# Kernel optimization log

Hardware: AMD Instinct MI355X
Metric: run time of the kernel (lower is better)

## Reference

```python
import jax, jax.numpy as jnp
import numpy as np

B, S, D = 4, 4096, 1024
H = 8                    # num_heads
DK = D // H              # head_k_dim = 128
DV = D // H              # head_v_dim = 128
KLEPE = 5                # lepe kernel size
ROPE_BASE = 10000.0


def rotate_half(x):
    x1, x2 = jnp.split(x, 2, axis=-1)
    return jnp.concatenate([-x2, x1], axis=-1)


def rope_sin_cos(seq_len, dim):
    inv_freq = 1.0 / (ROPE_BASE ** (jnp.arange(0, dim, 2, dtype=jnp.float32) / dim))
    freqs = jnp.arange(seq_len, dtype=jnp.float32)[:, None] * inv_freq[None, :]
    emb = jnp.concatenate([freqs, freqs], axis=-1)  # [S, dim]
    return jnp.sin(emb), jnp.cos(emb)


def mala_attn(q, k, v):
    """Magnitude-aware linear attention with inline RoPE.

    Attention weights A_ij = (scale*q_i.k_j + 1) / (scale*q_i.(sum_j k_j) + S):
    rows sum to 1 but, unlike plain linear attention, the sharpness of the
    distribution still depends on ||q_i|| (magnitude rectification). Computed
    in O(S*d^2) linear form without materializing the SxS matrix.
    q, k: [B,S,H,DK]; v: [B,S,H,DV].
    """
    sin, cos = rope_sin_cos(q.shape[1], q.shape[-1])
    sin, cos = sin[None, :, None, :], cos[None, :, None, :]
    q = q * cos + rotate_half(q) * sin
    k = k * cos + rotate_half(k) * sin
    scale = q.shape[-1] ** -0.5
    seq_len = q.shape[1]
    kv = jnp.einsum('bshd,bshe->bhde', k, v)      # [B,H,DK,DV]
    ksum = k.sum(axis=1)                          # [B,H,DK]
    vsum = v.sum(axis=1)                          # [B,H,DV]
    num = jnp.einsum('bshd,bhde->bshe', q, kv) * scale + vsum[:, None, :, :]
    den = jnp.einsum('bshd,bhd->bsh', q, ksum) * scale + seq_len
    return num / den[..., None]


def lepe_conv(v, w, b):
    # depthwise Conv1d over the sequence axis; channel id = h*DV + d
    Bb, Ss = v.shape[0], v.shape[1]
    x = v.transpose(0, 2, 3, 1).reshape(Bb, H * DV, Ss)   # [B, C, S]
    y = jax.lax.conv_general_dilated(
        x, w, window_strides=(1,), padding=[(KLEPE // 2, KLEPE // 2)],
        dimension_numbers=('NCH', 'OIH', 'NCH'), feature_group_count=H * DV)
    y = y + b[None, :, None]
    return y.reshape(Bb, H, DV, Ss).transpose(0, 3, 1, 2)  # [B,S,H,DV]


def setup_inputs() -> dict:
    key = jax.random.key(0)
    ks = jax.random.split(key, 8)
    w = 0.02
    return {
        'hidden_states': jax.random.normal(ks[0], (B, S, D), dtype=jnp.float32),
        'Wq': jax.random.normal(ks[1], (D, D), dtype=jnp.float32) * w,
        'Wk': jax.random.normal(ks[2], (D, D), dtype=jnp.float32) * w,
        'Wv': jax.random.normal(ks[3], (D, D), dtype=jnp.float32) * w,
        'Wg': jax.random.normal(ks[4], (D, D), dtype=jnp.float32) * w,
        'Wo': jax.random.normal(ks[5], (D, D), dtype=jnp.float32) * w,
        'lepe_w': jax.random.normal(ks[6], (D, 1, KLEPE), dtype=jnp.float32) * 0.1,
        'lepe_b': jnp.zeros((D,), dtype=jnp.float32),
    }


def reference(hidden_states, Wq, Wk, Wv, Wg, Wo, lepe_w, lepe_b):
    Bb, Ss, _ = hidden_states.shape
    q = (hidden_states @ Wq.T).reshape(Bb, Ss, H, DK)
    k = (hidden_states @ Wk.T).reshape(Bb, Ss, H, DK)
    v = (hidden_states @ Wv.T).reshape(Bb, Ss, H, DV)
    o_gate = hidden_states @ Wg.T                          # [B,S,D]
    o = mala_attn(q, k, v) + lepe_conv(v, lepe_w, lepe_b)  # [B,S,H,DV]
    o = o.reshape(Bb, Ss, H * DV) * o_gate
    return o @ Wo.T
```

## Files before the change

kernel.cpp:

```cpp
#include <hip/hip_runtime.h>
#include <math.h>
#include <stdint.h>


typedef __bf16 bf16;
typedef __bf16 bf16x2 __attribute__((ext_vector_type(2)));
typedef __bf16 bf16x4 __attribute__((ext_vector_type(4)));
typedef __bf16 bf16x8 __attribute__((ext_vector_type(8)));
typedef float f32x4 __attribute__((ext_vector_type(4)));

static constexpr float kScale = 0.08838834764831845f;

__device__ __forceinline__ void async_copy16(const void* g, void* l) {
  __builtin_amdgcn_global_load_lds(
      (const __attribute__((address_space(1))) void*)(uintptr_t)g,
      (__attribute__((address_space(3))) void*)(uintptr_t)l, 16, 0, 0);
}

__global__ __launch_bounds__(512, 1) void gemm_qkvg(
    const bf16* __restrict__ A, const bf16* __restrict__ Bw,
    bf16* __restrict__ C, const float2* __restrict__ tab)
{
  __shared__ __align__(16) char smem[131072];

  const int t = threadIdx.x;
  const int bid = blockIdx.x;
  const int n = bid >> 3;
  const int bx = (bid & 7) * 8 + (n & 7);
  const int by = n >> 3;
  const long m0 = (long)bx * 256;
  const long n0 = (long)by * 256;

  const int d0 = t * 16;
  const int dd = d0 ^ (((d0 >> 7) & 7) << 4);
  const int rT = dd >> 7;
  const int cT = (dd & 127) >> 1;
  const bf16* aSt = A  + (m0 + rT) * 1024 + cT;
  const bf16* bSt = Bw + (n0 + rT) * 1024 + cT;
  char* ldsDst = smem + d0;

  const int lane = t & 63, wid = t >> 6;
  const int wm = wid >> 2, wn = wid & 3;
  const int fm = lane & 15, fq = lane >> 4;
  const int xsw = (fm & 7) << 4;
  const int o0 = (fq * 16) ^ xsw;
  const int o1 = o0 ^ 64;
  const char* ldsA0 = smem + wm * 16384 + fm * 128 + o0;
  const char* ldsA1 = smem + wm * 16384 + fm * 128 + o1;
  const char* ldsB0 = smem + 32768 + (wn >> 1) * 16384 +
                      ((wn & 1) * 64 + fm) * 128 + o0;
  const char* ldsB1 = ldsB0 + (o1 - o0);

  f32x4 acc[8][4] = {};
  bf16x8 a4[4][2], b4[4][2];

#define STAGE_A(kt, h) do {                                                  \
    const bf16* s_ = aSt + (long)(h) * 131072 + (kt) * 64;                   \
    char* d_ = ldsDst + ((kt) & 1) * 65536 + (h) * 16384;                    \
    async_copy16(s_, d_);                                                    \
    async_copy16(s_ + 65536, d_ + 8192);                                     \
  } while (0)
#define STAGE_B(kt, h) do {                                                  \
    const bf16* s_ = bSt + (long)(h) * 131072 + (kt) * 64;                   \
    char* d_ = ldsDst + ((kt) & 1) * 65536 + 32768 + (h) * 16384;            \
    async_copy16(s_, d_);                                                    \
    async_copy16(s_ + 65536, d_ + 8192);                                     \
  } while (0)
#define LOAD_A(buf, qi) do {                                                 \
    const char* p0_ = ldsA0 + (buf) * 65536 + (qi) * 8192;                   \
    const char* p1_ = ldsA1 + (buf) * 65536 + (qi) * 8192;                   \
    a4[0][0] = *(const bf16x8*)(p0_);                                        \
    a4[0][1] = *(const bf16x8*)(p1_);                                        \
    a4[1][0] = *(const bf16x8*)(p0_ + 2048);                                 \
    a4[1][1] = *(const bf16x8*)(p1_ + 2048);                                 \
    a4[2][0] = *(const bf16x8*)(p0_ + 4096);                                 \
    a4[2][1] = *(const bf16x8*)(p1_ + 4096);                                 \
    a4[3][0] = *(const bf16x8*)(p0_ + 6144);                                 \
    a4[3][1] = *(const bf16x8*)(p1_ + 6144);                                 \
  } while (0)
#define LOAD_B(buf, qj) do {                                                 \
    const char* p0_ = ldsB0 + (buf) * 65536 + (qj) * 4096;                   \
    const char* p1_ = ldsB1 + (buf) * 65536 + (qj) * 4096;                   \
    b4[2*(qj)+0][0] = *(const bf16x8*)(p0_);                                 \
    b4[2*(qj)+0][1] = *(const bf16x8*)(p1_);                                 \
    b4[2*(qj)+1][0] = *(const bf16x8*)(p0_ + 2048);                          \
    b4[2*(qj)+1][1] = *(const bf16x8*)(p1_ + 2048);                          \
  } while (0)
#define MM1(i, j, ks)                                                        \
    acc[i][j] = __builtin_amdgcn_mfma_f32_16x16x32_bf16(                     \
        a4[(i) & 3][ks], b4[j][ks], acc[i][j], 0, 0, 0)
#define MFMA_Q(qi, qj) do {                                                  \
    MM1(4*(qi)+0, 2*(qj)+0, 0); MM1(4*(qi)+1, 2*(qj)+0, 0);                  \
    MM1(4*(qi)+2, 2*(qj)+0, 0); MM1(4*(qi)+3, 2*(qj)+0, 0);                  \
    MM1(4*(qi)+0, 2*(qj)+1, 0); MM1(4*(qi)+1, 2*(qj)+1, 0);                  \
    MM1(4*(qi)+2, 2*(qj)+1, 0); MM1(4*(qi)+3, 2*(qj)+1, 0);                  \
    MM1(4*(qi)+0, 2*(qj)+0, 1); MM1(4*(qi)+1, 2*(qj)+0, 1);                  \
    MM1(4*(qi)+2, 2*(qj)+0, 1); MM1(4*(qi)+3, 2*(qj)+0, 1);                  \
    MM1(4*(qi)+0, 2*(qj)+1, 1); MM1(4*(qi)+1, 2*(qj)+1, 1);                  \
    MM1(4*(qi)+2, 2*(qj)+1, 1); MM1(4*(qi)+3, 2*(qj)+1, 1);                  \
  } while (0)
#define BAR()    __builtin_amdgcn_s_barrier()
#define SCHEDB() __builtin_amdgcn_sched_barrier(0)
#define PRIO(p)  __builtin_amdgcn_s_setprio(p)

  STAGE_A(0, 0); STAGE_A(0, 1); STAGE_B(0, 0); STAGE_B(0, 1);
  STAGE_B(1, 0); STAGE_B(1, 1); STAGE_A(1, 0); STAGE_A(1, 1);
  asm volatile("s_waitcnt vmcnt(8)" ::: "memory");
  BAR(); SCHEDB();

#pragma unroll 1
  for (int it = 0; it < 7; ++it) {
    const int k2 = 2 * it + 2;
    const int k3 = 2 * it + 3;
    LOAD_A(0, 0); LOAD_B(0, 0);
    BAR(); SCHEDB(); PRIO(1); MFMA_Q(0, 0); PRIO(0); BAR(); SCHEDB();
    LOAD_B(0, 1);
    BAR(); SCHEDB(); PRIO(1); MFMA_Q(0, 1); PRIO(0); BAR(); SCHEDB();
    LOAD_A(0, 1);
    STAGE_B(k2, 0);
    BAR(); SCHEDB(); PRIO(1); MFMA_Q(1, 1); PRIO(0); BAR(); SCHEDB();
    STAGE_B(k2, 1); STAGE_A(k2, 0); STAGE_A(k2, 1);
    BAR(); SCHEDB(); PRIO(1); MFMA_Q(1, 0); PRIO(0);
    asm volatile("s_waitcnt vmcnt(8)" ::: "memory");
    BAR(); SCHEDB();
    LOAD_A(1, 0); LOAD_B(1, 0);
    BAR(); SCHEDB(); PRIO(1); MFMA_Q(0, 0); PRIO(0); BAR(); SCHEDB();
    LOAD_B(1, 1);
    BAR(); SCHEDB(); PRIO(1); MFMA_Q(0, 1); PRIO(0); BAR(); SCHEDB();
    LOAD_A(1, 1);
    STAGE_B(k3, 0);
    BAR(); SCHEDB(); PRIO(1); MFMA_Q(1, 1); PRIO(0); BAR(); SCHEDB();
    STAGE_B(k3, 1); STAGE_A(k3, 0); STAGE_A(k3, 1);
    BAR(); SCHEDB(); PRIO(1); MFMA_Q(1, 0); PRIO(0);
    asm volatile("s_waitcnt vmcnt(8)" ::: "memory");
    BAR(); SCHEDB();
  }

  {
    LOAD_A(0, 0); LOAD_B(0, 0);
    BAR(); SCHEDB(); PRIO(1); MFMA_Q(0, 0); PRIO(0); BAR(); SCHEDB();
    LOAD_B(0, 1);
    BAR(); SCHEDB(); PRIO(1); MFMA_Q(0, 1); PRIO(0); BAR(); SCHEDB();
    LOAD_A(0, 1);
    BAR(); SCHEDB(); PRIO(1); MFMA_Q(1, 1); PRIO(0); BAR(); SCHEDB();
    BAR(); SCHEDB(); PRIO(1); MFMA_Q(1, 0); PRIO(0);
    asm volatile("s_waitcnt vmcnt(0)" ::: "memory");
    BAR(); SCHEDB();
    LOAD_A(1, 0); LOAD_B(1, 0);
    BAR(); SCHEDB(); PRIO(1); MFMA_Q(0, 0); PRIO(0); BAR(); SCHEDB();
    LOAD_B(1, 1);
    BAR(); SCHEDB(); PRIO(1); MFMA_Q(0, 1); PRIO(0); BAR(); SCHEDB();
    LOAD_A(1, 1);
    BAR(); SCHEDB(); PRIO(1); MFMA_Q(1, 1); PRIO(0); BAR(); SCHEDB();
    BAR(); SCHEDB(); PRIO(1); MFMA_Q(1, 0); PRIO(0); BAR(); SCHEDB();
  }

#undef STAGE_A
#undef STAGE_B
#undef LOAD_A
#undef LOAD_B
#undef MM1
#undef MFMA_Q
#undef BAR
#undef SCHEDB
#undef PRIO

  bf16* T = (bf16*)smem;
  __syncthreads();
#pragma unroll 1
  for (int hw = 0; hw < 2; ++hw) {
    if (wm == hw) {
#pragma unroll
      for (int rf = 0; rf < 8; ++rf)
#pragma unroll
        for (int cf = 0; cf < 4; ++cf)
#pragma unroll
          for (int r = 0; r < 4; ++r)
            T[(rf * 16 + fq * 4 + r) * 264 + wn * 64 + cf * 16 + fm] =
                (bf16)acc[rf][cf][r];
    }
    __syncthreads();
    if (by < 8) {
#pragma unroll
      for (int ii = 0; ii < 32; ++ii) {
        const int pi = t + ii * 512;
        const int row = pi >> 7, pr = pi & 127;
        const int hd = pr >> 6, i = pr & 63;
        const int c0 = hd * 128 + i;
        const int s = (int)((m0 + hw * 128 + row) & 4095);
        const float2 sc = tab[s * 64 + i];
        float x1 = (float)T[row * 264 + c0];
        float x2 = (float)T[row * 264 + c0 + 64];
        T[row * 264 + c0]      = (bf16)(x1 * sc.y - x2 * sc.x);
        T[row * 264 + c0 + 64] = (bf16)(x2 * sc.y + x1 * sc.x);
      }
      __syncthreads();
    }
#pragma unroll
    for (int ii = 0; ii < 8; ++ii) {
      const int cid = t + ii * 512;
      const int row = cid >> 5, ch = cid & 31;
      *(bf16x8*)(C + (m0 + hw * 128 + row) * 4096 + n0 + ch * 8) =
          *(const bf16x8*)(T + row * 264 + ch * 8);
    }
    __syncthreads();
  }
}

__global__ __launch_bounds__(256, 2) void gemm_final(
    const bf16* __restrict__ A, const bf16* __restrict__ Bw,
    float* __restrict__ C)
{
  __shared__ __align__(16) bf16 As[128 * 32];
  __shared__ __align__(16) bf16 Bs[128 * 32];
  const int t = threadIdx.x;
  const int bid = blockIdx.x;
  const int xcd = bid & 7, n = bid >> 3;
  const int bx = xcd * 16 + (n & 15);
  const int by = n >> 4;
  const long m0 = (long)bx * 128;
  A  += m0 * 1024;
  Bw += (long)by * 131072;
  C  += m0 * 1024 + (long)by * 128;

  const int i0 = t, i1 = t + 256;
  const bf16* gA0 = A  + (long)(i0 >> 2) * 1024 + (i0 & 3) * 8;
  const bf16* gA1 = A  + (long)(i1 >> 2) * 1024 + (i1 & 3) * 8;
  const bf16* gB0 = Bw + (long)(i0 >> 2) * 1024 + (i0 & 3) * 8;
  const bf16* gB1 = Bw + (long)(i1 >> 2) * 1024 + (i1 & 3) * 8;
  bf16* lA0 = As + i0 * 8; bf16* lA1 = As + i1 * 8;
  bf16* lB0 = Bs + i0 * 8; bf16* lB1 = Bs + i1 * 8;

  const int lane = t & 63, wv = t >> 6;
  const int moff = (wv & 1) * 64, noff = (wv >> 1) * 64;
  const int fm = lane & 15, fq = lane >> 4;

  f32x4 acc[4][4] = {};

  for (int k0 = 0; k0 < 1024; k0 += 32) {
    async_copy16(gA0, lA0); async_copy16(gA1, lA1);
    async_copy16(gB0, lB0); async_copy16(gB1, lB1);
    gA0 += 32; gA1 += 32; gB0 += 32; gB1 += 32;
    __syncthreads();
    bf16x8 af[4], bfv[4];
#pragma unroll
    for (int i = 0; i < 4; ++i) {
      af[i]  = *(const bf16x8*)(As + (moff + i * 16 + fm) * 32 + fq * 8);
      bfv[i] = *(const bf16x8*)(Bs + (noff + i * 16 + fm) * 32 + fq * 8);
    }
#pragma unroll
    for (int i = 0; i < 4; ++i)
#pragma unroll
      for (int j = 0; j < 4; ++j)
        acc[i][j] = __builtin_amdgcn_mfma_f32_16x16x32_bf16(af[i], bfv[j], acc[i][j], 0, 0, 0);
    __syncthreads();
  }

#pragma unroll
  for (int i = 0; i < 4; ++i)
#pragma unroll
    for (int j = 0; j < 4; ++j)
#pragma unroll
      for (int r = 0; r < 4; ++r)
        C[(long)(moff + i * 16 + fq * 4 + r) * 1024 + noff + j * 16 + fm] = acc[i][j][r];
}

__global__ __launch_bounds__(256, 2) void gemm_num(
    const bf16* __restrict__ QKVG, const bf16* __restrict__ kvTall,
    const float* __restrict__ ksum, const float* __restrict__ vsum,
    const float* __restrict__ lepe_w, const float* __restrict__ lepe_b,
    bf16* __restrict__ obuf)
{
  __shared__ __align__(16) char smem[17408];
  bf16* As = (bf16*)smem;
  bf16* Bs = (bf16*)(smem + 8192);
  bf16* T  = (bf16*)smem;
  __shared__ float sden[128], svsum[128], slb[128], sksum[128];
  __shared__ float slw[5][128];

  const int t = threadIdx.x;
  const int h = blockIdx.y, b = blockIdx.z;
  const int bh = b * 8 + h;
  const long m0 = (long)blockIdx.x * 128;
  const bf16* A  = QKVG + (long)b * 16777216 + m0 * 4096 + h * 128;
  const bf16* Bw = kvTall + (long)bh * 16384;

  if (t < 128) {
    sksum[t] = ksum[bh * 128 + t];
    svsum[t] = vsum[bh * 128 + t];
    slb[t]   = lepe_b[h * 128 + t];
#pragma unroll
    for (int j = 0; j < 5; ++j) slw[j][t] = lepe_w[(h * 128 + t) * 5 + j];
  }

  const int i0 = t, i1 = t + 256;
  const bf16* gA0 = A + (long)(i0 >> 2) * 4096 + (i0 & 3) * 8;
  const bf16* gA1 = A + (long)(i1 >> 2) * 4096 + (i1 & 3) * 8;
  const bf16* gB0 = Bw + (long)(i0 >> 2) * 128 + (i0 & 3) * 8;
  const bf16* gB1 = Bw + (long)(i1 >> 2) * 128 + (i1 & 3) * 8;
  bf16* lA0 = As + i0 * 8; bf16* lA1 = As + i1 * 8;
  bf16* lB0 = Bs + i0 * 8; bf16* lB1 = Bs + i1 * 8;

  const int lane = t & 63, wv = t >> 6;
  const int moff = (wv & 1) * 64, noff = (wv >> 1) * 64;
  const int fm = lane & 15, fq = lane >> 4;

  f32x4 acc[4][4] = {};
  float dacc = 0.f;

  for (int k0 = 0; k0 < 128; k0 += 32) {
    async_copy16(gA0, lA0); async_copy16(gA1, lA1);
    async_copy16(gB0, lB0); async_copy16(gB1, lB1);
    gA0 += 32; gA1 += 32; gB0 += 32; gB1 += 32;
    __syncthreads();
    bf16x8 af[4], bfv[4];
#pragma unroll
    for (int i = 0; i < 4; ++i) {
      af[i]  = *(const bf16x8*)(As + (moff + i * 16 + fm) * 32 + fq * 8);
      bfv[i] = *(const bf16x8*)(Bs + (noff + i * 16 + fm) * 32 + fq * 8);
    }
#pragma unroll
    for (int i = 0; i < 4; ++i)
#pragma unroll
      for (int j = 0; j < 4; ++j)
        acc[i][j] = __builtin_amdgcn_mfma_f32_16x16x32_bf16(af[i], bfv[j], acc[i][j], 0, 0, 0);
    if (t < 128) {
#pragma unroll
      for (int c8 = 0; c8 < 4; ++c8) {
        bf16x8 q8 = *(const bf16x8*)(As + t * 32 + c8 * 8);
#pragma unroll
        for (int e = 0; e < 8; ++e) dacc += (float)q8[e] * sksum[k0 + c8 * 8 + e];
      }
    }
    __syncthreads();
  }
  if (t < 128) sden[t] = dacc * kScale + 4096.0f;

  const int c2 = lane * 2;
  const float w0[5] = {slw[0][c2], slw[1][c2], slw[2][c2], slw[3][c2], slw[4][c2]};
  const float w1[5] = {slw[0][c2+1], slw[1][c2+1], slw[2][c2+1], slw[3][c2+1], slw[4][c2+1]};
  const float lb0 = slb[c2], lb1 = slb[c2 + 1];

#pragma unroll
  for (int half = 0; half < 2; ++half) {
    if ((wv & 1) == half) {
#pragma unroll
      for (int i = 0; i < 4; ++i)
#pragma unroll
        for (int j = 0; j < 4; ++j)
#pragma unroll
          for (int r = 0; r < 4; ++r) {
            const int col = noff + j * 16 + fm;
            T[(i * 16 + fq * 4 + r) * 136 + col] = (bf16)(acc[i][j][r] * kScale + svsum[col]);
          }
    }
    __syncthreads();
    for (int rr = 0; rr < 16; ++rr) {
      const int lrow = wv * 16 + rr;
      const int row = half * 64 + lrow;
      const int s = (int)(m0 + row);
      const long grow = (long)b * 4096 + s;
      const float rden = 1.0f / sden[row];
      const bf16* vrow = QKVG + grow * 4096 + 2048 + h * 128 + c2;
      bf16x2 a2 = *(const bf16x2*)(T + lrow * 136 + c2);
      float lep0 = lb0, lep1 = lb1;
#pragma unroll
      for (int jt = 0; jt < 5; ++jt) {
        const int srow = s + jt - 2;
        if (srow >= 0 && srow < 4096) {
          bf16x2 v2 = *(const bf16x2*)(vrow + (long)(jt - 2) * 4096);
          lep0 += (float)v2[0] * w0[jt];
          lep1 += (float)v2[1] * w1[jt];
        }
      }
      bf16x2 g2 = *(const bf16x2*)(QKVG + grow * 4096 + 3072 + h * 128 + c2);
      bf16x2 o2;
      o2[0] = (bf16)(((float)a2[0] * rden + lep0) * (float)g2[0]);
      o2[1] = (bf16)(((float)a2[1] * rden + lep1) * (float)g2[1]);
      *(bf16x2*)(obuf + grow * 1024 + h * 128 + c2) = o2;
    }
    __syncthreads();
  }
}

__global__ void prep_kernel(const float* __restrict__ X, const float* __restrict__ Wq,
                            const float* __restrict__ Wk, const float* __restrict__ Wv,
                            const float* __restrict__ Wg, const float* __restrict__ Wo,
                            bf16* __restrict__ Xb, bf16* __restrict__ Wcat,
                            bf16* __restrict__ Wob, float2* __restrict__ tab)
{
  const int blk = blockIdx.x;
  if (blk < 16384) {
    long g = ((long)blk * 256 + threadIdx.x) * 4;
    float4 v = *(const float4*)(X + g);
    bf16x4 o = {(bf16)v.x, (bf16)v.y, (bf16)v.z, (bf16)v.w};
    *(bf16x4*)(Xb + g) = o;
  } else if (blk < 21504) {
    long g = ((long)(blk - 16384) * 256 + threadIdx.x) * 4;
    if (g < 4194304) {
      long idx = g & 1048575;
      int sel = (int)(g >> 20);
      const float* s = sel == 0 ? Wq : sel == 1 ? Wk : sel == 2 ? Wv : Wg;
      float4 v = *(const float4*)(s + idx);
      bf16x4 o = {(bf16)v.x, (bf16)v.y, (bf16)v.z, (bf16)v.w};
      *(bf16x4*)(Wcat + g) = o;
    } else {
      long idx = g - 4194304;
      float4 v = *(const float4*)(Wo + idx);
      bf16x4 o = {(bf16)v.x, (bf16)v.y, (bf16)v.z, (bf16)v.w};
      *(bf16x4*)(Wob + idx) = o;
    }
  } else {
    int idx = (blk - 21504) * 256 + threadIdx.x;
    int s = idx >> 6, i = idx & 63;
    float inv = powf(10000.0f, -((float)(2 * i)) / 128.0f);
    float ang = (float)s * inv;
    float sn, cs;
    sincosf(ang, &sn, &cs);
    tab[idx] = make_float2(sn, cs);
  }
}

__global__ __launch_bounds__(256, 2) void kv_mfma(
    const bf16* __restrict__ QKVG, float* __restrict__ kvp,
    float* __restrict__ ksump, float* __restrict__ vsump)
{
  __shared__ __align__(16) bf16 VT[128 * 40];
  __shared__ __align__(16) bf16 KT[128 * 40];
  const int t = threadIdx.x;
  const int chunk = blockIdx.x, bh = blockIdx.y;
  const int b = bh >> 3, h = bh & 7;
  const long rowbase = ((long)b * 4096 + chunk * 256) * 4096 + h * 128;
  const bf16* Kg = QKVG + rowbase + 1024;
  const bf16* Vg = QKVG + rowbase + 2048;

  const int sp = t >> 4, fc = t & 15;
  const int lane = t & 63, wv = t >> 6;
  const int eoff = (wv & 1) * 64, doff = (wv >> 1) * 64;
  const int fm = lane & 15, fq = lane >> 4;
  const int srow = t & 127;
  const bool sumK = t >= 128;

  f32x4 acc[4][4] = {};
  float rsum = 0.f;

  for (int sb = 0; sb < 256; sb += 32) {
    const long go = (long)(sb + 2 * sp) * 4096 + fc * 8;
    bf16x8 v0 = *(const bf16x8*)(Vg + go);
    bf16x8 v1 = *(const bf16x8*)(Vg + go + 4096);
    bf16x8 k0 = *(const bf16x8*)(Kg + go);
    bf16x8 k1 = *(const bf16x8*)(Kg + go + 4096);
#pragma unroll
    for (int j = 0; j < 8; ++j) {
      const int f = fc * 8 + j;
      bf16x2 vp2 = {v0[j], v1[j]};
      bf16x2 kp2 = {k0[j], k1[j]};
      *(bf16x2*)(VT + f * 40 + 2 * sp) = vp2;
      *(bf16x2*)(KT + f * 40 + 2 * sp) = kp2;
    }
    __syncthreads();
    bf16x8 af[4], bfv[4];
#pragma unroll
    for (int i = 0; i < 4; ++i) {
      af[i]  = *(const bf16x8*)(VT + (eoff + i * 16 + fm) * 40 + fq * 8);
      bfv[i] = *(const bf16x8*)(KT + (doff + i * 16 + fm) * 40 + fq * 8);
    }
#pragma unroll
    for (int i = 0; i < 4; ++i)
#pragma unroll
      for (int j = 0; j < 4; ++j)
        acc[i][j] = __builtin_amdgcn_mfma_f32_16x16x32_bf16(af[i], bfv[j], acc[i][j], 0, 0, 0);
    const bf16* rp = (sumK ? KT : VT) + srow * 40;
#pragma unroll
    for (int i = 0; i < 4; ++i) {
      bf16x8 r8 = *(const bf16x8*)(rp + i * 8);
#pragma unroll
      for (int j = 0; j < 8; ++j) rsum += (float)r8[j];
    }
    __syncthreads();
  }

  float* plane = kvp + ((long)chunk * 32 + bh) * 16384;
#pragma unroll
  for (int i = 0; i < 4; ++i)
#pragma unroll
    for (int j = 0; j < 4; ++j)
#pragma unroll
      for (int r = 0; r < 4; ++r)
        plane[(long)(eoff + i * 16 + fq * 4 + r) * 128 + (doff + j * 16 + fm)] = acc[i][j][r];
  float* sdst = (sumK ? ksump : vsump) + ((long)chunk * 32 + bh) * 128 + srow;
  *sdst = rsum;
}

__global__ void kv_reduce(const float* __restrict__ kvp, const float* __restrict__ ksump,
                          const float* __restrict__ vsump, bf16* __restrict__ kvT,
                          float* __restrict__ ksum, float* __restrict__ vsum)
{
  long g = (long)blockIdx.x * 256 + threadIdx.x;
  long bh = g >> 14, idx = g & 16383;
  float s = 0.f;
#pragma unroll
  for (int c = 0; c < 16; ++c) s += kvp[((long)c * 32 + bh) * 16384 + idx];
  kvT[g] = (bf16)s;
  if (g < 8192) {
    int bh2 = (int)(g >> 8), rem = (int)(g & 255), f = rem & 127;
    const float* src = (rem >> 7) ? ksump : vsump;
    float* dst = (rem >> 7) ? ksum : vsum;
    float s2 = 0.f;
#pragma unroll
    for (int c = 0; c < 16; ++c) s2 += src[((long)c * 32 + bh2) * 128 + f];
    dst[bh2 * 128 + f] = s2;
  }
}

extern "C" void kernel_launch(void* const* d_in, const int* in_sizes, int n_in,
                              void* d_out, int out_size, void* d_ws, size_t ws_size,
                              hipStream_t stream)
{
  const float* X      = (const float*)d_in[0];
  const float* Wq     = (const float*)d_in[1];
  const float* Wk     = (const float*)d_in[2];
  const float* Wv     = (const float*)d_in[3];
  const float* Wg     = (const float*)d_in[4];
  const float* Wo     = (const float*)d_in[5];
  const float* lepe_w = (const float*)d_in[6];
  const float* lepe_b = (const float*)d_in[7];
  float* out = (float*)d_out;

  char* ws = (char*)d_ws;
  bf16*   Xb    = (bf16*)(ws);
  float*  kvp   = (float*)(ws);
  bf16*   Wcat  = (bf16*)(ws + 33554432);
  bf16*   Wob   = (bf16*)(ws + 41943040);
  float2* tab   = (float2*)(ws + 44040192);
  float*  ksump = (float*)(ws + 44040192);
  float*  vsump = (float*)(ws + 44302336);
  bf16*   QKVG  = (bf16*)(ws + 46137344);
  float*  ksum  = (float*)(ws + 180355072);
  float*  vsum  = (float*)(ws + 180371456);
  bf16*   kvT   = (bf16*)(ws + 180387840);
  bf16*   obuf  = (bf16*)(ws + 181960704);

  prep_kernel<<<22528, 256, 0, stream>>>(X, Wq, Wk, Wv, Wg, Wo, Xb, Wcat, Wob, tab);

  gemm_qkvg<<<1024, 512, 0, stream>>>(Xb, Wcat, QKVG, tab);

  kv_mfma<<<dim3(16, 32), 256, 0, stream>>>(QKVG, kvp, ksump, vsump);
  kv_reduce<<<2048, 256, 0, stream>>>(kvp, ksump, vsump, kvT, ksum, vsum);

  gemm_num<<<dim3(32, 8, 4), 256, 0, stream>>>(QKVG, kvT, ksum, vsum, lepe_w, lepe_b, obuf);

  gemm_final<<<1024, 256, 0, stream>>>(obuf, Wob, out);
}
```

Measured before the change: 432.1 us.

## Restructure QKVG GEMM main loop with separate A-fragment registers and fewer barriers

```diff
diff --git a/kernel.cpp b/kernel.cpp
--- a/kernel.cpp
+++ b/kernel.cpp
@@ -52,7 +52,7 @@
   const char* ldsB1 = ldsB0 + (o1 - o0);
 
   f32x4 acc[8][4] = {};
-  bf16x8 a4[4][2], b4[4][2];
+  bf16x8 aLo[4][2], aHi[4][2], b4[4][2];
 
 #define STAGE_A(kt, h) do {                                                  \
     const bf16* s_ = aSt + (long)(h) * 131072 + (kt) * 64;                   \
@@ -66,17 +66,17 @@
     async_copy16(s_, d_);                                                    \
     async_copy16(s_ + 65536, d_ + 8192);                                     \
   } while (0)
-#define LOAD_A(buf, qi) do {                                                 \
+#define LOAD_A(dst, buf, qi) do {                                            \
     const char* p0_ = ldsA0 + (buf) * 65536 + (qi) * 8192;                   \
     const char* p1_ = ldsA1 + (buf) * 65536 + (qi) * 8192;                   \
-    a4[0][0] = *(const bf16x8*)(p0_);                                        \
-    a4[0][1] = *(const bf16x8*)(p1_);                                        \
-    a4[1][0] = *(const bf16x8*)(p0_ + 2048);                                 \
-    a4[1][1] = *(const bf16x8*)(p1_ + 2048);                                 \
-    a4[2][0] = *(const bf16x8*)(p0_ + 4096);                                 \
-    a4[2][1] = *(const bf16x8*)(p1_ + 4096);                                 \
-    a4[3][0] = *(const bf16x8*)(p0_ + 6144);                                 \
-    a4[3][1] = *(const bf16x8*)(p1_ + 6144);                                 \
+    dst[0][0] = *(const bf16x8*)(p0_);                                       \
+    dst[0][1] = *(const bf16x8*)(p1_);                                       \
+    dst[1][0] = *(const bf16x8*)(p0_ + 2048);                                \
+    dst[1][1] = *(const bf16x8*)(p1_ + 2048);                                \
+    dst[2][0] = *(const bf16x8*)(p0_ + 4096);                                \
+    dst[2][1] = *(const bf16x8*)(p1_ + 4096);                                \
+    dst[3][0] = *(const bf16x8*)(p0_ + 6144);                                \
+    dst[3][1] = *(const bf16x8*)(p1_ + 6144);                                \
   } while (0)
 #define LOAD_B(buf, qj) do {                                                 \
     const char* p0_ = ldsB0 + (buf) * 65536 + (qj) * 4096;                   \
@@ -86,22 +86,32 @@
     b4[2*(qj)+1][0] = *(const bf16x8*)(p0_ + 2048);                          \
     b4[2*(qj)+1][1] = *(const bf16x8*)(p1_ + 2048);                          \
   } while (0)
-#define MM1(i, j, ks)                                                        \
+#define MM1(arr, i, j, ks)                                                   \
     acc[i][j] = __builtin_amdgcn_mfma_f32_16x16x32_bf16(                     \
-        a4[(i) & 3][ks], b4[j][ks], acc[i][j], 0, 0, 0)
-#define MFMA_Q(qi, qj) do {                                                  \
-    MM1(4*(qi)+0, 2*(qj)+0, 0); MM1(4*(qi)+1, 2*(qj)+0, 0);                  \
-    MM1(4*(qi)+2, 2*(qj)+0, 0); MM1(4*(qi)+3, 2*(qj)+0, 0);                  \
-    MM1(4*(qi)+0, 2*(qj)+1, 0); MM1(4*(qi)+1, 2*(qj)+1, 0);                  \
-    MM1(4*(qi)+2, 2*(qj)+1, 0); MM1(4*(qi)+3, 2*(qj)+1, 0);                  \
-    MM1(4*(qi)+0, 2*(qj)+0, 1); MM1(4*(qi)+1, 2*(qj)+0, 1);                  \
-    MM1(4*(qi)+2, 2*(qj)+0, 1); MM1(4*(qi)+3, 2*(qj)+0, 1);                  \
-    MM1(4*(qi)+0, 2*(qj)+1, 1); MM1(4*(qi)+1, 2*(qj)+1, 1);                  \
-    MM1(4*(qi)+2, 2*(qj)+1, 1); MM1(4*(qi)+3, 2*(qj)+1, 1);                  \
+        arr[(i) & 3][ks], b4[j][ks], acc[i][j], 0, 0, 0)
+#define MFMA_Q(arr, qi, qj) do {                                             \
+    MM1(arr, 4*(qi)+0, 2*(qj)+0, 0); MM1(arr, 4*(qi)+1, 2*(qj)+0, 0);        \
+    MM1(arr, 4*(qi)+2, 2*(qj)+0, 0); MM1(arr, 4*(qi)+3, 2*(qj)+0, 0);        \
+    MM1(arr, 4*(qi)+0, 2*(qj)+1, 0); MM1(arr, 4*(qi)+1, 2*(qj)+1, 0);        \
+    MM1(arr, 4*(qi)+2, 2*(qj)+1, 0); MM1(arr, 4*(qi)+3, 2*(qj)+1, 0);        \
+    MM1(arr, 4*(qi)+0, 2*(qj)+0, 1); MM1(arr, 4*(qi)+1, 2*(qj)+0, 1);        \
+    MM1(arr, 4*(qi)+2, 2*(qj)+0, 1); MM1(arr, 4*(qi)+3, 2*(qj)+0, 1);        \
+    MM1(arr, 4*(qi)+0, 2*(qj)+1, 1); MM1(arr, 4*(qi)+1, 2*(qj)+1, 1);        \
+    MM1(arr, 4*(qi)+2, 2*(qj)+1, 1); MM1(arr, 4*(qi)+3, 2*(qj)+1, 1);        \
   } while (0)
 #define BAR()    __builtin_amdgcn_s_barrier()
 #define SCHEDB() __builtin_amdgcn_sched_barrier(0)
 #define PRIO(p)  __builtin_amdgcn_s_setprio(p)
+#define TILE_HEAD(buf) do {                                                  \
+    LOAD_A(aLo, buf, 0);                                                     \
+    LOAD_B(buf, 0); LOAD_B(buf, 1);                                          \
+    LOAD_A(aHi, buf, 1);                                                     \
+    PRIO(1);                                                                 \
+    MFMA_Q(aLo, 0, 0); MFMA_Q(aLo, 0, 1); MFMA_Q(aHi, 1, 1);                 \
+    PRIO(0);                                                                 \
+    asm volatile("s_waitcnt lgkmcnt(0)" ::: "memory");                       \
+    BAR(); SCHEDB();                                                         \
+  } while (0)
 
   STAGE_A(0, 0); STAGE_A(0, 1); STAGE_B(0, 0); STAGE_B(0, 1);
   STAGE_B(1, 0); STAGE_B(1, 1); STAGE_A(1, 0); STAGE_A(1, 1);
@@ -112,48 +122,26 @@
   for (int it = 0; it < 7; ++it) {
     const int k2 = 2 * it + 2;
     const int k3 = 2 * it + 3;
-    LOAD_A(0, 0); LOAD_B(0, 0);
-    BAR(); SCHEDB(); PRIO(1); MFMA_Q(0, 0); PRIO(0); BAR(); SCHEDB();
-    LOAD_B(0, 1);
-    BAR(); SCHEDB(); PRIO(1); MFMA_Q(0, 1); PRIO(0); BAR(); SCHEDB();
-    LOAD_A(0, 1);
-    STAGE_B(k2, 0);
-    BAR(); SCHEDB(); PRIO(1); MFMA_Q(1, 1); PRIO(0); BAR(); SCHEDB();
-    STAGE_B(k2, 1); STAGE_A(k2, 0); STAGE_A(k2, 1);
-    BAR(); SCHEDB(); PRIO(1); MFMA_Q(1, 0); PRIO(0);
+    TILE_HEAD(0);
+    STAGE_B(k2, 0); STAGE_B(k2, 1); STAGE_A(k2, 0); STAGE_A(k2, 1);
+    SCHEDB();
+    PRIO(1); MFMA_Q(aHi, 1, 0); PRIO(0);
     asm volatile("s_waitcnt vmcnt(8)" ::: "memory");
     BAR(); SCHEDB();
-    LOAD_A(1, 0); LOAD_B(1, 0);
-    BAR(); SCHEDB(); PRIO(1); MFMA_Q(0, 0); PRIO(0); BAR(); SCHEDB();
-    LOAD_B(1, 1);
-    BAR(); SCHEDB(); PRIO(1); MFMA_Q(0, 1); PRIO(0); BAR(); SCHEDB();
-    LOAD_A(1, 1);
-    STAGE_B(k3, 0);
-    BAR(); SCHEDB(); PRIO(1); MFMA_Q(1, 1); PRIO(0); BAR(); SCHEDB();
-    STAGE_B(k3, 1); STAGE_A(k3, 0); STAGE_A(k3, 1);
-    BAR(); SCHEDB(); PRIO(1); MFMA_Q(1, 0); PRIO(0);
+    TILE_HEAD(1);
+    STAGE_B(k3, 0); STAGE_B(k3, 1); STAGE_A(k3, 0); STAGE_A(k3, 1);
+    SCHEDB();
+    PRIO(1); MFMA_Q(aHi, 1, 0); PRIO(0);
     asm volatile("s_waitcnt vmcnt(8)" ::: "memory");
     BAR(); SCHEDB();
   }
 
-  {
-    LOAD_A(0, 0); LOAD_B(0, 0);
-    BAR(); SCHEDB(); PRIO(1); MFMA_Q(0, 0); PRIO(0); BAR(); SCHEDB();
-    LOAD_B(0, 1);
-    BAR(); SCHEDB(); PRIO(1); MFMA_Q(0, 1); PRIO(0); BAR(); SCHEDB();
-    LOAD_A(0, 1);
-    BAR(); SCHEDB(); PRIO(1); MFMA_Q(1, 1); PRIO(0); BAR(); SCHEDB();
-    BAR(); SCHEDB(); PRIO(1); MFMA_Q(1, 0); PRIO(0);
-    asm volatile("s_waitcnt vmcnt(0)" ::: "memory");
-    BAR(); SCHEDB();
-    LOAD_A(1, 0); LOAD_B(1, 0);
-    BAR(); SCHEDB(); PRIO(1); MFMA_Q(0, 0); PRIO(0); BAR(); SCHEDB();
-    LOAD_B(1, 1);
-    BAR(); SCHEDB(); PRIO(1); MFMA_Q(0, 1); PRIO(0); BAR(); SCHEDB();
-    LOAD_A(1, 1);
-    BAR(); SCHEDB(); PRIO(1); MFMA_Q(1, 1); PRIO(0); BAR(); SCHEDB();
-    BAR(); SCHEDB(); PRIO(1); MFMA_Q(1, 0); PRIO(0); BAR(); SCHEDB();
-  }
+  TILE_HEAD(0);
+  PRIO(1); MFMA_Q(aHi, 1, 0); PRIO(0);
+  asm volatile("s_waitcnt vmcnt(0)" ::: "memory");
+  BAR(); SCHEDB();
+  TILE_HEAD(1);
+  PRIO(1); MFMA_Q(aHi, 1, 0); PRIO(0);
 
 #undef STAGE_A
 #undef STAGE_B
@@ -161,6 +149,7 @@
 #undef LOAD_B
 #undef MM1
 #undef MFMA_Q
+#undef TILE_HEAD
 #undef BAR
 #undef SCHEDB
 #undef PRIO
```

Result: no change. 431.8 us (-0.1%).
